# Kernel optimization log

Hardware: AMD Instinct MI355X
Metric: run time of the kernel (lower is better)

Reference implementation:

```python
import jax, jax.numpy as jnp
import numpy as np
import math

B, S, D, H = 4, 2048, 1024, 16
HD = D // H  # head_dim = 64


def setup_inputs() -> dict:
    key = jax.random.key(0)
    ks = jax.random.split(key, 7)
    s = 0.02
    return {
        "q": jax.random.normal(ks[0], (B, S, D), jnp.float32),
        "k": jax.random.normal(ks[1], (B, S, D), jnp.float32),
        "v": jax.random.normal(ks[2], (B, S, D), jnp.float32),
        "wq": jax.random.normal(ks[3], (D, D), jnp.float32) * s,
        "wk": jax.random.normal(ks[4], (D, D), jnp.float32) * s,
        "wv": jax.random.normal(ks[5], (D, D), jnp.float32) * s,
        "wo": jax.random.normal(ks[6], (D, D), jnp.float32) * s,
    }


def reference(q, k, v, wq, wk, wv, wo):
    # Linear (no bias): y = x @ W.T, W is (out, in)
    xq = jnp.einsum('bsd,ed->bse', q, wq).reshape(B, S, H, HD).transpose(0, 2, 1, 3)
    xk = jnp.einsum('bsd,ed->bse', k, wk).reshape(B, S, H, HD).transpose(0, 2, 1, 3)
    xv = jnp.einsum('bsd,ed->bse', v, wv).reshape(B, S, H, HD).transpose(0, 2, 1, 3)
    scores = jnp.einsum('bhqd,bhkd->bhqk', xq, xk) / math.sqrt(HD)  # [B,H,S,S]
    causal = jnp.tril(jnp.ones((S, S), dtype=bool))
    scores = jnp.where(causal[None, None], scores, jnp.float32(-jnp.inf))
    probs = jax.nn.softmax(scores, axis=-1)  # dropout p=0 -> identity
    out = jnp.einsum('bhqk,bhkd->bhqd', probs, xv)  # [B,H,S,HD]
    out = out.transpose(0, 2, 1, 3).reshape(B, S, D)
    return jnp.einsum('bsd,ed->bse', out, wo)
```

## Files before the change

### kernel.cpp

```cpp
#include <hip/hip_runtime.h>

#define SS 2048
#define DD 1024
#define HH 16
#define HD 64
#define MM 8192

typedef unsigned short ushort_t;
typedef __attribute__((ext_vector_type(8))) short short8;
typedef __attribute__((ext_vector_type(4))) float f32x4;
typedef __attribute__((ext_vector_type(4))) unsigned short us4;
typedef __attribute__((ext_vector_type(8))) unsigned short us8;

__device__ __forceinline__ ushort_t f2bf(float f) {
    union { float f; unsigned u; } x; x.f = f;
    unsigned r = x.u + 0x7fffu + ((x.u >> 16) & 1u);
    return (ushort_t)(r >> 16);
}
__device__ __forceinline__ float bf2f(ushort_t h) {
    union { unsigned u; float f; } x; x.u = ((unsigned)h) << 16; return x.f;
}
__device__ __forceinline__ unsigned pack_bf2(float a, float b) {
    union { float f; unsigned u; } x, y; x.f = a; y.f = b;
    return __builtin_amdgcn_perm(y.u, x.u, 0x07060302u);
}

__device__ __forceinline__ void async16(const void* g, void* l) {
    __builtin_amdgcn_global_load_lds(
        (const __attribute__((address_space(1))) unsigned int*)g,
        (__attribute__((address_space(3))) unsigned int*)l, 16, 0, 0);
}

__global__ void cvt_all(const float* __restrict__ q, const float* __restrict__ k,
                        const float* __restrict__ v, const float* __restrict__ wq,
                        const float* __restrict__ wk, const float* __restrict__ wv,
                        const float* __restrict__ wo, ushort_t* __restrict__ qbf,
                        ushort_t* __restrict__ kbf, ushort_t* __restrict__ vbf,
                        ushort_t* __restrict__ wbf) {
    long i = ((long)blockIdx.x * 256 + threadIdx.x) * 8;
    const float* src; ushort_t* dst;
    if (i < (3l << 23)) {
        int s = (int)(i >> 23);
        long off = i & ((1l << 23) - 1);
        src = ((s == 0) ? q : (s == 1) ? k : v) + off;
        dst = ((s == 0) ? qbf : (s == 1) ? kbf : vbf) + off;
    } else {
        long j = i - (3l << 23);
        int s = (int)(j >> 20);
        src = ((s == 0) ? wq : (s == 1) ? wk : (s == 2) ? wv : wo) + (j & 1048575);
        dst = wbf + j;
    }
    float4 f0 = *(const float4*)src;
    float4 f1 = *(const float4*)(src + 4);
    us8 o;
    o[0] = f2bf(f0.x); o[1] = f2bf(f0.y); o[2] = f2bf(f0.z); o[3] = f2bf(f0.w);
    o[4] = f2bf(f1.x); o[5] = f2bf(f1.y); o[6] = f2bf(f1.z); o[7] = f2bf(f1.w);
    *(us8*)dst = o;
}

__device__ __forceinline__ void epi_scatter(f32x4 acc[4][4], int m0, int n0,
                                            int mode, void* Yv) {
    int tid = threadIdx.x;
    int w = tid >> 6, lane = tid & 63;
    int l16 = lane & 15, quad = lane >> 4;
    int wm = (w >> 1) * 64, wn = (w & 1) * 64;
    #pragma unroll
    for (int mt = 0; mt < 4; ++mt) {
        #pragma unroll
        for (int r = 0; r < 4; ++r) {
            int row = m0 + wm + mt * 16 + quad * 4 + r;
            #pragma unroll
            for (int nt = 0; nt < 4; ++nt) {
                int col = n0 + wn + nt * 16 + l16;
                float vf = acc[mt][nt][r];
                if (mode == 2) {
                    ((float*)Yv)[(size_t)row * DD + col] = vf;
                } else {
                    ushort_t vh = f2bf(vf);
                    int b = row >> 11, s = row & 2047;
                    int h = col >> 6,  hd = col & 63;
                    if (mode == 0) {
                        ((ushort_t*)Yv)[(((size_t)b * HH + h) * SS + s) * HD + hd] = vh;
                    } else {
                        int sp = (s & ~63) | (((s & 15) << 2) | ((s >> 4) & 3));
                        ((ushort_t*)Yv)[(((size_t)b * HH + h) * HD + hd) * SS + sp] = vh;
                    }
                }
            }
        }
    }
}

__global__ __launch_bounds__(256) void proj3f(const ushort_t* __restrict__ qbf,
                                              const ushort_t* __restrict__ kbf,
                                              const ushort_t* __restrict__ vbf,
                                              const ushort_t* __restrict__ Wall,
                                              ushort_t* __restrict__ xq,
                                              ushort_t* __restrict__ xk,
                                              ushort_t* __restrict__ xvT) {
    __shared__ __align__(16) ushort_t As[3][128 * 32];
    __shared__ __align__(16) ushort_t Bs[3][128 * 32];
    int tid = threadIdx.x;
    int w = tid >> 6, lane = tid & 63;
    int l16 = lane & 15, quad = lane >> 4;
    int mat   = (int)(blockIdx.x >> 9);
    int inner = (int)(blockIdx.x & 511);
    int m0 = (inner & 63) * 128;
    int n0 = (inner >> 6) * 128;
    const ushort_t* A  = (mat == 0) ? qbf : (mat == 1) ? kbf : vbf;
    const ushort_t* Bw = Wall + ((size_t)mat << 20);
    int wm = (w >> 1) * 64, wn = (w & 1) * 64;

    f32x4 acc[4][4];
    #pragma unroll
    for (int i = 0; i < 4; ++i)
        #pragma unroll
        for (int j = 0; j < 4; ++j) acc[i][j] = (f32x4){0.f, 0.f, 0.f, 0.f};

    int g0 = w * 64 + lane, r0 = g0 >> 2, j0 = ((g0 & 3) ^ (r0 & 3)) * 8;
    int g1 = g0 + 256,      r1 = g1 >> 2, j1 = ((g1 & 3) ^ (r1 & 3)) * 8;
    int swA = (quad ^ (l16 & 3)) * 8;

    const ushort_t* Ar0 = A  + (size_t)(m0 + r0) * DD + j0;
    const ushort_t* Ar1 = A  + (size_t)(m0 + r1) * DD + j1;
    const ushort_t* Br0 = Bw + (size_t)(n0 + r0) * DD + j0;
    const ushort_t* Br1 = Bw + (size_t)(n0 + r1) * DD + j1;
    int ldsA0 = w * 64 * 8, ldsA1 = (256 + w * 64) * 8;

    async16(Ar0,      &As[0][ldsA0]);
    async16(Ar1,      &As[0][ldsA1]);
    async16(Br0,      &Bs[0][ldsA0]);
    async16(Br1,      &Bs[0][ldsA1]);
    async16(Ar0 + 32, &As[1][ldsA0]);
    async16(Ar1 + 32, &As[1][ldsA1]);
    async16(Br0 + 32, &Bs[1][ldsA0]);
    async16(Br1 + 32, &Bs[1][ldsA1]);

    int c = 0, c2 = 2;
    for (int kk = 0; kk < 32; ++kk) {
        __builtin_amdgcn_s_barrier();
        if (kk < 30) {
            int k2 = (kk + 2) * 32;
            async16(Ar0 + k2, &As[c2][ldsA0]);
            async16(Ar1 + k2, &As[c2][ldsA1]);
            async16(Br0 + k2, &Bs[c2][ldsA0]);
            async16(Br1 + k2, &Bs[c2][ldsA1]);
            asm volatile("s_waitcnt vmcnt(8)" ::: "memory");
        } else if (kk == 30) {
            asm volatile("s_waitcnt vmcnt(4)" ::: "memory");
        } else {
            asm volatile("s_waitcnt vmcnt(0)" ::: "memory");
        }
        __builtin_amdgcn_s_barrier();
        __builtin_amdgcn_sched_barrier(0);

        short8 af[4], bfr[4];
        #pragma unroll
        for (int t = 0; t < 4; ++t) {
            af[t]  = *(const short8*)&As[c][(wm + t * 16 + l16) * 32 + swA];
            bfr[t] = *(const short8*)&Bs[c][(wn + t * 16 + l16) * 32 + swA];
        }
        #pragma unroll
        for (int mt = 0; mt < 4; ++mt)
            #pragma unroll
            for (int nt = 0; nt < 4; ++nt)
                acc[mt][nt] = __builtin_amdgcn_mfma_f32_16x16x32_bf16(af[mt], bfr[nt], acc[mt][nt], 0, 0, 0);

        c  = (c  == 2) ? 0 : c  + 1;
        c2 = (c2 == 2) ? 0 : c2 + 1;
    }

    void* Y = (mat == 0) ? (void*)xq : (mat == 1) ? (void*)xk : (void*)xvT;
    epi_scatter(acc, m0, n0, (mat == 2) ? 1 : 0, Y);
}

__global__ __launch_bounds__(512) void out_gemm(const ushort_t* __restrict__ Abf,
                                                const ushort_t* __restrict__ Bw,
                                                float* __restrict__ Y) {
    __shared__ __align__(16) ushort_t As[2][256 * 32];
    __shared__ __align__(16) ushort_t Bs[2][128 * 32];
    int tid = threadIdx.x;
    int w = tid >> 6, lane = tid & 63;
    int l16 = lane & 15, quad = lane >> 4;
    int inner = (int)blockIdx.x;
    int m0 = (inner & 31) * 256;
    int n0 = (inner >> 5) * 128;
    int wm = (w >> 1) * 64, wn = (w & 1) * 64;

    f32x4 acc[4][4];
    #pragma unroll
    for (int i = 0; i < 4; ++i)
        #pragma unroll
        for (int j = 0; j < 4; ++j) acc[i][j] = (f32x4){0.f, 0.f, 0.f, 0.f};

    int ra0 = tid >> 2,           ja0 = ((tid & 3) ^ (ra0 & 3)) * 8;
    int ga1 = tid + 512;
    int ra1 = ga1 >> 2,           ja1 = ((ga1 & 3) ^ (ra1 & 3)) * 8;
    int rb  = tid >> 2,           jb  = ((tid & 3) ^ (rb & 3)) * 8;
    int swA = (quad ^ (l16 & 3)) * 8;

    async16(Abf + (size_t)(m0 + ra0) * DD + ja0, &As[0][(size_t)(w * 64) * 8]);
    async16(Abf + (size_t)(m0 + ra1) * DD + ja1, &As[0][(size_t)(512 + w * 64) * 8]);
    async16(Bw  + (size_t)(n0 + rb)  * DD + jb,  &Bs[0][(size_t)(w * 64) * 8]);

    for (int kk = 0; kk < 32; ++kk) {
        int c = kk & 1;
        __syncthreads();
        if (kk < 31) {
            int k1 = (kk + 1) * 32;
            async16(Abf + (size_t)(m0 + ra0) * DD + k1 + ja0, &As[c ^ 1][(size_t)(w * 64) * 8]);
            async16(Abf + (size_t)(m0 + ra1) * DD + k1 + ja1, &As[c ^ 1][(size_t)(512 + w * 64) * 8]);
            async16(Bw  + (size_t)(n0 + rb)  * DD + k1 + jb,  &Bs[c ^ 1][(size_t)(w * 64) * 8]);
        }
        short8 af[4], bfr[4];
        #pragma unroll
        for (int t = 0; t < 4; ++t) {
            af[t]  = *(const short8*)&As[c][(wm + t * 16 + l16) * 32 + swA];
            bfr[t] = *(const short8*)&Bs[c][(wn + t * 16 + l16) * 32 + swA];
        }
        #pragma unroll
        for (int mt = 0; mt < 4; ++mt)
            #pragma unroll
            for (int nt = 0; nt < 4; ++nt)
                acc[mt][nt] = __builtin_amdgcn_mfma_f32_16x16x32_bf16(af[mt], bfr[nt], acc[mt][nt], 0, 0, 0);
    }
    epi_scatter(acc, m0, n0, 2, Y);
}

__global__ __launch_bounds__(512) void attn_kernel(const ushort_t* __restrict__ xq,
                                                   const ushort_t* __restrict__ xk,
                                                   const ushort_t* __restrict__ xvT,
                                                   ushort_t* __restrict__ ao) {
    __shared__ __align__(16) ushort_t Ksm[2][64 * 64];
    __shared__ __align__(16) ushort_t Vsm[2][64 * 64];
    __shared__ __align__(16) ushort_t Psm[8][16 * 72];

    int tid = threadIdx.x;
    int w = tid >> 6, lane = tid & 63;
    int l16 = lane & 15, quad = lane >> 4;
    int bh = blockIdx.x & 63;
    int p  = blockIdx.x >> 6;
    int b = bh >> 4, h = bh & 15;

    const ushort_t* Q  = xq  + (size_t)bh * SS * HD;
    const ushort_t* K  = xk  + (size_t)bh * SS * HD;
    const ushort_t* VT = xvT + (size_t)bh * HD * SS;

    int r0 = tid >> 3, j0 = ((tid & 7) ^ (r0 & 7)) * 8;
    int ldsb = (w * 64) * 8;

    short8 ones;
    #pragma unroll
    for (int i = 0; i < 8; ++i) ones[i] = (short)0x3F80;

    const float CS = 0.125f * 1.44269504f;

    for (int ph = 0; ph < 2; ++ph) {
        int qt = ph ? (15 - p) : p;
        int qb = qt * 128;
        int qmin = qb + w * 16;
        int ktmax = 2 * qt + 1;

        short8 aq[2];
        #pragma unroll
        for (int kc = 0; kc < 2; ++kc) {
            short8 t = *(const short8*)(Q + (size_t)(qmin + l16) * HD + kc * 32 + quad * 8);
            #pragma unroll
            for (int i = 0; i < 8; ++i)
                t[i] = (short)f2bf(bf2f((ushort_t)t[i]) * CS);
            aq[kc] = t;
        }

        f32x4 o[4];
        #pragma unroll
        for (int dt = 0; dt < 4; ++dt) o[dt] = (f32x4){0.f, 0.f, 0.f, 0.f};
        f32x4 lacc = (f32x4){0.f, 0.f, 0.f, 0.f};

        __syncthreads();
        async16(K  + (size_t)r0 * HD + j0, &Ksm[0][ldsb]);
        async16(VT + (size_t)r0 * SS + j0, &Vsm[0][ldsb]);

        for (int kt = 0; kt <= ktmax; ++kt) {
            int kb = kt * 64;
            int c = kt & 1;
            __syncthreads();
            if (kt < ktmax) {
                int kb1 = kb + 64;
                async16(K  + (size_t)(kb1 + r0) * HD + j0, &Ksm[c ^ 1][ldsb]);
                async16(VT + (size_t)r0 * SS + kb1 + j0, &Vsm[c ^ 1][ldsb]);
            }

            f32x4 sc[4];
            __builtin_amdgcn_s_setprio(1);
            #pragma unroll
            for (int nt = 0; nt < 4; ++nt) {
                int row = nt * 16 + l16;
                short8 bk0 = *(const short8*)&Ksm[c][row * 64 + ((0 + quad) ^ (l16 & 7)) * 8];
                short8 bk1 = *(const short8*)&Ksm[c][row * 64 + ((4 + quad) ^ (l16 & 7)) * 8];
                f32x4 cc = (f32x4){0.f, 0.f, 0.f, 0.f};
                cc = __builtin_amdgcn_mfma_f32_16x16x32_bf16(aq[0], bk0, cc, 0, 0, 0);
                cc = __builtin_amdgcn_mfma_f32_16x16x32_bf16(aq[1], bk1, cc, 0, 0, 0);
                sc[nt] = cc;
            }
            __builtin_amdgcn_s_setprio(0);

            bool msk = (kb + 63 > qmin);
            #pragma unroll
            for (int r = 0; r < 4; ++r) {
                float e0, e1, e2, e3;
                if (msk) {
                    int qg = qmin + quad * 4 + r;
                    e0 = (kb +  0 + l16 <= qg) ? __builtin_amdgcn_exp2f(sc[0][r]) : 0.f;
                    e1 = (kb + 16 + l16 <= qg) ? __builtin_amdgcn_exp2f(sc[1][r]) : 0.f;
                    e2 = (kb + 32 + l16 <= qg) ? __builtin_amdgcn_exp2f(sc[2][r]) : 0.f;
                    e3 = (kb + 48 + l16 <= qg) ? __builtin_amdgcn_exp2f(sc[3][r]) : 0.f;
                } else {
                    e0 = __builtin_amdgcn_exp2f(sc[0][r]);
                    e1 = __builtin_amdgcn_exp2f(sc[1][r]);
                    e2 = __builtin_amdgcn_exp2f(sc[2][r]);
                    e3 = __builtin_amdgcn_exp2f(sc[3][r]);
                }
                uint2 pk = { pack_bf2(e0, e1), pack_bf2(e2, e3) };
                *(uint2*)&Psm[w][(quad * 4 + r) * 72 + l16 * 4] = pk;
            }

            asm volatile("s_waitcnt lgkmcnt(0)" ::: "memory");

            __builtin_amdgcn_s_setprio(1);
            #pragma unroll
            for (int kc = 0; kc < 2; ++kc) {
                short8 ap = *(const short8*)&Psm[w][l16 * 72 + kc * 32 + quad * 8];
                lacc = __builtin_amdgcn_mfma_f32_16x16x32_bf16(ap, ones, lacc, 0, 0, 0);
                #pragma unroll
                for (int dt = 0; dt < 4; ++dt) {
                    int row = dt * 16 + l16;
                    short8 bv = *(const short8*)&Vsm[c][row * 64 + ((kc * 4 + quad) ^ (l16 & 7)) * 8];
                    o[dt] = __builtin_amdgcn_mfma_f32_16x16x32_bf16(ap, bv, o[dt], 0, 0, 0);
                }
            }
            __builtin_amdgcn_s_setprio(0);
        }

        #pragma unroll
        for (int r = 0; r < 4; ++r) {
            float inv = 1.0f / lacc[r];
            int qg = qmin + quad * 4 + r;
            #pragma unroll
            for (int dt = 0; dt < 4; ++dt)
                ao[((size_t)(b * SS + qg)) * DD + h * HD + dt * 16 + l16] = f2bf(o[dt][r] * inv);
        }
    }
}

extern "C" void kernel_launch(void* const* d_in, const int* in_sizes, int n_in,
                              void* d_out, int out_size, void* d_ws, size_t ws_size,
                              hipStream_t stream) {
    const float* q  = (const float*)d_in[0];
    const float* k  = (const float*)d_in[1];
    const float* v  = (const float*)d_in[2];
    const float* wq = (const float*)d_in[3];
    const float* wk = (const float*)d_in[4];
    const float* wv = (const float*)d_in[5];
    const float* wo = (const float*)d_in[6];
    float* out = (float*)d_out;

    ushort_t* wbf = (ushort_t*)d_ws;
    ushort_t* xq  = wbf + 4194304ull;
    ushort_t* xk  = xq  + 8388608ull;
    ushort_t* xvT = xk  + 8388608ull;
    ushort_t* ao  = xvT + 8388608ull;
    ushort_t* vbf = ao;
    ushort_t* qbf = (ushort_t*)d_out;
    ushort_t* kbf = qbf + 8388608ull;

    cvt_all<<<14336, 256, 0, stream>>>(q, k, v, wq, wk, wv, wo, qbf, kbf, vbf, wbf);
    proj3f<<<1536, 256, 0, stream>>>(qbf, kbf, vbf, wbf, xq, xk, xvT);
    attn_kernel<<<512, 512, 0, stream>>>(xq, xk, xvT, ao);
    out_gemm<<<256, 512, 0, stream>>>(ao, wbf + 3145728ull, out);
}
```

Before: 324.0 us.

## Load K and V tiles directly from global into registers per wave

Removes the shared-memory double-buffered K/V staging with async copies and block barriers, and instead has each wave load its K and V MFMA operands straight from global memory into registers. This drops all __syncthreads in the inner loop and frees LDS. The cost is that each of the 8 waves reloads the same K/V tile from global/L2 instead of sharing one LDS copy, which multiplies cache traffic. There is also no prefetch of the next tile, so global load latency is exposed every iteration.

New measurement: 509.9 us. 1.57x slower.

```diff
diff --git a/kernel.cpp b/kernel.cpp
--- a/kernel.cpp
+++ b/kernel.cpp
@@ -231,8 +231,6 @@
                                                    const ushort_t* __restrict__ xk,
                                                    const ushort_t* __restrict__ xvT,
                                                    ushort_t* __restrict__ ao) {
-    __shared__ __align__(16) ushort_t Ksm[2][64 * 64];
-    __shared__ __align__(16) ushort_t Vsm[2][64 * 64];
     __shared__ __align__(16) ushort_t Psm[8][16 * 72];
 
     int tid = threadIdx.x;
@@ -246,9 +244,6 @@
     const ushort_t* K  = xk  + (size_t)bh * SS * HD;
     const ushort_t* VT = xvT + (size_t)bh * HD * SS;
 
-    int r0 = tid >> 3, j0 = ((tid & 7) ^ (r0 & 7)) * 8;
-    int ldsb = (w * 64) * 8;
-
     short8 ones;
     #pragma unroll
     for (int i = 0; i < 8; ++i) ones[i] = (short)0x3F80;
@@ -276,33 +271,35 @@
         for (int dt = 0; dt < 4; ++dt) o[dt] = (f32x4){0.f, 0.f, 0.f, 0.f};
         f32x4 lacc = (f32x4){0.f, 0.f, 0.f, 0.f};
 
-        __syncthreads();
-        async16(K  + (size_t)r0 * HD + j0, &Ksm[0][ldsb]);
-        async16(VT + (size_t)r0 * SS + j0, &Vsm[0][ldsb]);
-
         for (int kt = 0; kt <= ktmax; ++kt) {
             int kb = kt * 64;
-            int c = kt & 1;
-            __syncthreads();
-            if (kt < ktmax) {
-                int kb1 = kb + 64;
-                async16(K  + (size_t)(kb1 + r0) * HD + j0, &Ksm[c ^ 1][ldsb]);
-                async16(VT + (size_t)r0 * SS + kb1 + j0, &Vsm[c ^ 1][ldsb]);
+
+            short8 bk0[4], bk1[4];
+            #pragma unroll
+            for (int nt = 0; nt < 4; ++nt) {
+                const ushort_t* kr = K + (size_t)(kb + nt * 16 + l16) * HD + quad * 8;
+                bk0[nt] = *(const short8*)(kr);
+                bk1[nt] = *(const short8*)(kr + 32);
             }
 
             f32x4 sc[4];
             __builtin_amdgcn_s_setprio(1);
             #pragma unroll
             for (int nt = 0; nt < 4; ++nt) {
-                int row = nt * 16 + l16;
-                short8 bk0 = *(const short8*)&Ksm[c][row * 64 + ((0 + quad) ^ (l16 & 7)) * 8];
-                short8 bk1 = *(const short8*)&Ksm[c][row * 64 + ((4 + quad) ^ (l16 & 7)) * 8];
                 f32x4 cc = (f32x4){0.f, 0.f, 0.f, 0.f};
-                cc = __builtin_amdgcn_mfma_f32_16x16x32_bf16(aq[0], bk0, cc, 0, 0, 0);
-                cc = __builtin_amdgcn_mfma_f32_16x16x32_bf16(aq[1], bk1, cc, 0, 0, 0);
+                cc = __builtin_amdgcn_mfma_f32_16x16x32_bf16(aq[0], bk0[nt], cc, 0, 0, 0);
+                cc = __builtin_amdgcn_mfma_f32_16x16x32_bf16(aq[1], bk1[nt], cc, 0, 0, 0);
                 sc[nt] = cc;
             }
             __builtin_amdgcn_s_setprio(0);
+
+            short8 bv[2][4];
+            #pragma unroll
+            for (int kc = 0; kc < 2; ++kc)
+                #pragma unroll
+                for (int dt = 0; dt < 4; ++dt)
+                    bv[kc][dt] = *(const short8*)(VT + (size_t)(dt * 16 + l16) * SS
+                                                  + kb + kc * 32 + quad * 8);
 
             bool msk = (kb + 63 > qmin);
             #pragma unroll
@@ -332,11 +329,8 @@
                 short8 ap = *(const short8*)&Psm[w][l16 * 72 + kc * 32 + quad * 8];
                 lacc = __builtin_amdgcn_mfma_f32_16x16x32_bf16(ap, ones, lacc, 0, 0, 0);
                 #pragma unroll
-                for (int dt = 0; dt < 4; ++dt) {
-                    int row = dt * 16 + l16;
-                    short8 bv = *(const short8*)&Vsm[c][row * 64 + ((kc * 4 + quad) ^ (l16 & 7)) * 8];
-                    o[dt] = __builtin_amdgcn_mfma_f32_16x16x32_bf16(ap, bv, o[dt], 0, 0, 0);
-                }
+                for (int dt = 0; dt < 4; ++dt)
+                    o[dt] = __builtin_amdgcn_mfma_f32_16x16x32_bf16(ap, bv[kc][dt], o[dt], 0, 0, 0);
             }
             __builtin_amdgcn_s_setprio(0);
         }
```

## Fuse fp32-to-bf16 activation conversion into projection GEMM loads

Applied to the files above, without the earlier changes.

The separate conversion pass for q/k/v activations is removed. The projection GEMM now streams fp32 activations directly into LDS and packs them to bf16 when loading fragments, so only the weights are pre-converted. This avoids writing and re-reading 3x8M bf16 intermediates. In exchange each GEMM tile reads twice the A bytes, the pipeline drops from triple to double buffering with a plain __syncthreads, and packing adds extra VALU work in the inner loop.

After: 354.3 us. +9.4%, slower.

```diff
diff --git a/kernel.cpp b/kernel.cpp
--- a/kernel.cpp
+++ b/kernel.cpp
@@ -31,31 +31,18 @@
         (__attribute__((address_space(3))) unsigned int*)l, 16, 0, 0);
 }
 
-__global__ void cvt_all(const float* __restrict__ q, const float* __restrict__ k,
-                        const float* __restrict__ v, const float* __restrict__ wq,
-                        const float* __restrict__ wk, const float* __restrict__ wv,
-                        const float* __restrict__ wo, ushort_t* __restrict__ qbf,
-                        ushort_t* __restrict__ kbf, ushort_t* __restrict__ vbf,
-                        ushort_t* __restrict__ wbf) {
-    long i = ((long)blockIdx.x * 256 + threadIdx.x) * 8;
-    const float* src; ushort_t* dst;
-    if (i < (3l << 23)) {
-        int s = (int)(i >> 23);
-        long off = i & ((1l << 23) - 1);
-        src = ((s == 0) ? q : (s == 1) ? k : v) + off;
-        dst = ((s == 0) ? qbf : (s == 1) ? kbf : vbf) + off;
-    } else {
-        long j = i - (3l << 23);
-        int s = (int)(j >> 20);
-        src = ((s == 0) ? wq : (s == 1) ? wk : (s == 2) ? wv : wo) + (j & 1048575);
-        dst = wbf + j;
-    }
-    float4 f0 = *(const float4*)src;
-    float4 f1 = *(const float4*)(src + 4);
+__global__ void cvt_w(const float* __restrict__ wq, const float* __restrict__ wk,
+                      const float* __restrict__ wv, const float* __restrict__ wo,
+                      ushort_t* __restrict__ dst) {
+    int i = (blockIdx.x * 256 + threadIdx.x) * 8;
+    int w = i >> 20, j = i & 1048575;
+    const float* src = (w == 0) ? wq : (w == 1) ? wk : (w == 2) ? wv : wo;
+    float4 f0 = *(const float4*)(src + j);
+    float4 f1 = *(const float4*)(src + j + 4);
     us8 o;
     o[0] = f2bf(f0.x); o[1] = f2bf(f0.y); o[2] = f2bf(f0.z); o[3] = f2bf(f0.w);
     o[4] = f2bf(f1.x); o[5] = f2bf(f1.y); o[6] = f2bf(f1.z); o[7] = f2bf(f1.w);
-    *(us8*)dst = o;
+    *(us8*)(dst + i) = o;
 }
 
 __device__ __forceinline__ void epi_scatter(f32x4 acc[4][4], int m0, int n0,
@@ -91,15 +78,15 @@
     }
 }
 
-__global__ __launch_bounds__(256) void proj3f(const ushort_t* __restrict__ qbf,
-                                              const ushort_t* __restrict__ kbf,
-                                              const ushort_t* __restrict__ vbf,
+__global__ __launch_bounds__(256) void proj3f(const float* __restrict__ q,
+                                              const float* __restrict__ k,
+                                              const float* __restrict__ v,
                                               const ushort_t* __restrict__ Wall,
                                               ushort_t* __restrict__ xq,
                                               ushort_t* __restrict__ xk,
                                               ushort_t* __restrict__ xvT) {
-    __shared__ __align__(16) ushort_t As[3][128 * 32];
-    __shared__ __align__(16) ushort_t Bs[3][128 * 32];
+    __shared__ __align__(16) ushort_t As[2][128 * 64];
+    __shared__ __align__(16) ushort_t Bs[2][128 * 32];
     int tid = threadIdx.x;
     int w = tid >> 6, lane = tid & 63;
     int l16 = lane & 15, quad = lane >> 4;
@@ -107,7 +94,7 @@
     int inner = (int)(blockIdx.x & 511);
     int m0 = (inner & 63) * 128;
     int n0 = (inner >> 6) * 128;
-    const ushort_t* A  = (mat == 0) ? qbf : (mat == 1) ? kbf : vbf;
+    const float*    A  = (mat == 0) ? q : (mat == 1) ? k : v;
     const ushort_t* Bw = Wall + ((size_t)mat << 20);
     int wm = (w >> 1) * 64, wn = (w & 1) * 64;
 
@@ -117,57 +104,57 @@
         #pragma unroll
         for (int j = 0; j < 4; ++j) acc[i][j] = (f32x4){0.f, 0.f, 0.f, 0.f};
 
-    int g0 = w * 64 + lane, r0 = g0 >> 2, j0 = ((g0 & 3) ^ (r0 & 3)) * 8;
-    int g1 = g0 + 256,      r1 = g1 >> 2, j1 = ((g1 & 3) ^ (r1 & 3)) * 8;
-    int swA = (quad ^ (l16 & 3)) * 8;
-
-    const ushort_t* Ar0 = A  + (size_t)(m0 + r0) * DD + j0;
-    const ushort_t* Ar1 = A  + (size_t)(m0 + r1) * DD + j1;
-    const ushort_t* Br0 = Bw + (size_t)(n0 + r0) * DD + j0;
-    const ushort_t* Br1 = Bw + (size_t)(n0 + r1) * DD + j1;
-    int ldsA0 = w * 64 * 8, ldsA1 = (256 + w * 64) * 8;
-
-    async16(Ar0,      &As[0][ldsA0]);
-    async16(Ar1,      &As[0][ldsA1]);
-    async16(Br0,      &Bs[0][ldsA0]);
-    async16(Br1,      &Bs[0][ldsA1]);
-    async16(Ar0 + 32, &As[1][ldsA0]);
-    async16(Ar1 + 32, &As[1][ldsA1]);
-    async16(Br0 + 32, &Bs[1][ldsA0]);
-    async16(Br1 + 32, &Bs[1][ldsA1]);
-
-    int c = 0, c2 = 2;
+    int ra[4], ca[4];
+    #pragma unroll
+    for (int kgi = 0; kgi < 4; ++kgi) {
+        int g = tid + 256 * kgi;
+        int r = g >> 3, gi = g & 7;
+        int gis = (((gi >> 1) ^ (r & 3)) << 1) | (gi & 1);
+        ra[kgi] = r; ca[kgi] = gis * 4;
+    }
+    int rb0 = tid >> 2,          jb0 = ((tid & 3) ^ (rb0 & 3)) * 8;
+    int gb1 = tid + 256;
+    int rb1 = gb1 >> 2,          jb1 = ((gb1 & 3) ^ (rb1 & 3)) * 8;
+    int swA = (quad ^ (l16 & 3)) * 16;
+    int swB = (quad ^ (l16 & 3)) * 8;
+
+    #pragma unroll
+    for (int kgi = 0; kgi < 4; ++kgi)
+        async16(A + (size_t)(m0 + ra[kgi]) * DD + ca[kgi], &As[0][(tid + 256 * kgi) * 8]);
+    async16(Bw + (size_t)(n0 + rb0) * DD + jb0, &Bs[0][(size_t)(w * 64) * 8]);
+    async16(Bw + (size_t)(n0 + rb1) * DD + jb1, &Bs[0][(size_t)(256 + w * 64) * 8]);
+
     for (int kk = 0; kk < 32; ++kk) {
-        __builtin_amdgcn_s_barrier();
-        if (kk < 30) {
-            int k2 = (kk + 2) * 32;
-            async16(Ar0 + k2, &As[c2][ldsA0]);
-            async16(Ar1 + k2, &As[c2][ldsA1]);
-            async16(Br0 + k2, &Bs[c2][ldsA0]);
-            async16(Br1 + k2, &Bs[c2][ldsA1]);
-            asm volatile("s_waitcnt vmcnt(8)" ::: "memory");
-        } else if (kk == 30) {
-            asm volatile("s_waitcnt vmcnt(4)" ::: "memory");
-        } else {
-            asm volatile("s_waitcnt vmcnt(0)" ::: "memory");
-        }
-        __builtin_amdgcn_s_barrier();
-        __builtin_amdgcn_sched_barrier(0);
-
+        int c = kk & 1;
+        __syncthreads();
+        if (kk < 31) {
+            int k1 = (kk + 1) * 32;
+            #pragma unroll
+            for (int kgi = 0; kgi < 4; ++kgi)
+                async16(A + (size_t)(m0 + ra[kgi]) * DD + k1 + ca[kgi],
+                        &As[c ^ 1][(tid + 256 * kgi) * 8]);
+            async16(Bw + (size_t)(n0 + rb0) * DD + k1 + jb0, &Bs[c ^ 1][(size_t)(w * 64) * 8]);
+            async16(Bw + (size_t)(n0 + rb1) * DD + k1 + jb1, &Bs[c ^ 1][(size_t)(256 + w * 64) * 8]);
+        }
         short8 af[4], bfr[4];
         #pragma unroll
         for (int t = 0; t < 4; ++t) {
-            af[t]  = *(const short8*)&As[c][(wm + t * 16 + l16) * 32 + swA];
-            bfr[t] = *(const short8*)&Bs[c][(wn + t * 16 + l16) * 32 + swA];
+            int rowA = (wm + t * 16 + l16) * 64 + swA;
+            f32x4 fa0 = *(const f32x4*)&As[c][rowA];
+            f32x4 fa1 = *(const f32x4*)&As[c][rowA + 8];
+            union { uint4 u; short8 s; } cv;
+            cv.u.x = pack_bf2(fa0[0], fa0[1]);
+            cv.u.y = pack_bf2(fa0[2], fa0[3]);
+            cv.u.z = pack_bf2(fa1[0], fa1[1]);
+            cv.u.w = pack_bf2(fa1[2], fa1[3]);
+            af[t]  = cv.s;
+            bfr[t] = *(const short8*)&Bs[c][(wn + t * 16 + l16) * 32 + swB];
         }
         #pragma unroll
         for (int mt = 0; mt < 4; ++mt)
             #pragma unroll
             for (int nt = 0; nt < 4; ++nt)
                 acc[mt][nt] = __builtin_amdgcn_mfma_f32_16x16x32_bf16(af[mt], bfr[nt], acc[mt][nt], 0, 0, 0);
-
-        c  = (c  == 2) ? 0 : c  + 1;
-        c2 = (c2 == 2) ? 0 : c2 + 1;
     }
 
     void* Y = (mat == 0) ? (void*)xq : (mat == 1) ? (void*)xk : (void*)xvT;
@@ -369,12 +356,9 @@
     ushort_t* xk  = xq  + 8388608ull;
     ushort_t* xvT = xk  + 8388608ull;
     ushort_t* ao  = xvT + 8388608ull;
-    ushort_t* vbf = ao;
-    ushort_t* qbf = (ushort_t*)d_out;
-    ushort_t* kbf = qbf + 8388608ull;
-
-    cvt_all<<<14336, 256, 0, stream>>>(q, k, v, wq, wk, wv, wo, qbf, kbf, vbf, wbf);
-    proj3f<<<1536, 256, 0, stream>>>(qbf, kbf, vbf, wbf, xq, xk, xvT);
+
+    cvt_w<<<2048, 256, 0, stream>>>(wq, wk, wv, wo, wbf);
+    proj3f<<<1536, 256, 0, stream>>>(q, k, v, wbf, xq, xk, xvT);
     attn_kernel<<<512, 512, 0, stream>>>(xq, xk, xvT, ao);
     out_gemm<<<256, 512, 0, stream>>>(ao, wbf + 3145728ull, out);
 }
```
